# Performance work log

Measured on AMD Instinct MI355X. Metric: run time of the kernel, lower is better.

The kernel has to match this reference:

```python
import jax, jax.numpy as jnp
import numpy as np

N = 100000      # nodes
E = 1000000     # edges (avg degree 10)
F_IN = 64       # num_features
HID = 64        # hidden_channels
C1 = 4          # num_labeled_classes
C2 = 3          # num_unlabeled_classes
L = 4           # num_layers
ALPHA = 0.1


def setup_inputs() -> dict:
    key = jax.random.key(0)
    ks = jax.random.split(key, 8)
    x = jax.random.normal(ks[0], (N, F_IN), dtype=jnp.float32)
    edge_index = jax.random.randint(ks[1], (2, E), 0, N, dtype=jnp.int32)
    # GCN2Conv shared weights (glorot-ish scale), one per residual layer
    Ws = jax.random.normal(ks[2], (L - 1, F_IN, F_IN), dtype=jnp.float32) / np.sqrt(F_IN)
    # GCNConv weight + bias
    W_gcn = jax.random.normal(ks[3], (F_IN, HID), dtype=jnp.float32) / np.sqrt(F_IN)
    b_gcn = jnp.zeros((HID,), dtype=jnp.float32)
    # classification heads
    W1 = jax.random.normal(ks[4], (HID, C1), dtype=jnp.float32) / np.sqrt(HID)
    b1 = jnp.zeros((C1,), dtype=jnp.float32)
    W2 = jax.random.normal(ks[5], (HID, C2), dtype=jnp.float32) / np.sqrt(HID)
    b2 = jnp.zeros((C2,), dtype=jnp.float32)
    return {"x": x, "edge_index": edge_index, "Ws": Ws, "W_gcn": W_gcn,
            "b_gcn": b_gcn, "W1": W1, "b1": b1, "W2": W2, "b2": b2}


def _gcn_norm(edge_index, num_nodes):
    # PyG gcn_norm: add self-loops, symmetric D^-1/2 A D^-1/2 normalization
    loop = jnp.arange(num_nodes, dtype=edge_index.dtype)
    row = jnp.concatenate([edge_index[0], loop])  # source
    col = jnp.concatenate([edge_index[1], loop])  # target
    deg = jax.ops.segment_sum(jnp.ones_like(col, dtype=jnp.float32), col,
                              num_segments=num_nodes)
    dinv = jnp.where(deg > 0, jax.lax.rsqrt(deg), 0.0)
    norm = dinv[row] * dinv[col]  # [E+N]
    return row, col, norm


def _propagate(x, row, col, norm, num_nodes):
    # out[col] += norm * x[row]  (gather -> scale -> scatter-add)
    return jax.ops.segment_sum(norm[:, None] * x[row], col, num_segments=num_nodes)


def reference(x, edge_index, Ws, W_gcn, b_gcn, W1, b1, W2, b2):
    num_nodes = x.shape[0]
    row, col, norm = _gcn_norm(edge_index, num_nodes)
    x0 = x
    # GCN2Conv layers: theta=None -> beta=1.0, shared weights ->
    # out = ((1-alpha) * A_hat x + alpha * x0) @ W
    for i in range(L - 1):
        h = _propagate(x, row, col, norm, num_nodes)
        h = (1.0 - ALPHA) * h + ALPHA * x0
        h = h @ Ws[i]
        x = jax.nn.relu(h)
        # dropout(p=0.5) is inactive in eval mode
        x0 = x  # repo updates x_0 each layer
    # GCNConv: A_hat (x W) + b
    h = _propagate(x @ W_gcn, row, col, norm, num_nodes) + b_gcn
    out1 = h @ W1 + b1  # l2_classifier is False
    out2 = h @ W2 + b2
    return out1, out2, h
```

## Files before the change

kernel.cpp:

```cpp
#include <hip/hip_runtime.h>
#include <hip/hip_bf16.h>


#define TPB 256
#define NBSH 7
typedef __hip_bfloat16 bf16;
typedef __attribute__((ext_vector_type(8))) short short8;
typedef __attribute__((ext_vector_type(4))) float f32x4;

#define MFMA16(A, B, C) __builtin_amdgcn_mfma_f32_16x16x32_bf16((A), (B), (C), 0, 0, 0)

__device__ __forceinline__ float lo16(int u) { return __int_as_float(u << 16); }
__device__ __forceinline__ float hi16(int u) { return __int_as_float(u & 0xffff0000); }

__device__ __forceinline__ unsigned f2bfu(float f) {
    unsigned x = __float_as_uint(f);
    return ((x + 0x7fffu + ((x >> 16) & 1u)) >> 16) & 0xffffu;
}

__global__ void ebhist_kernel(const int* __restrict__ col, int* __restrict__ bh,
                              int E, int B) {
    __shared__ int lh[800];
    for (int i = threadIdx.x; i < B; i += blockDim.x) lh[i] = 0;
    __syncthreads();
    for (int e = blockIdx.x * blockDim.x + threadIdx.x; e < E; e += gridDim.x * blockDim.x)
        atomicAdd(&lh[col[e] >> NBSH], 1);
    __syncthreads();
    for (int i = threadIdx.x; i < B; i += blockDim.x) {
        int c = lh[i];
        if (c) atomicAdd(&bh[i], c);
    }
}

__global__ void bscan_kernel(const int* __restrict__ bh, int* __restrict__ bcur,
                             int* __restrict__ boff, int B, int E) {
    __shared__ int s[256];
    int t = threadIdx.x;
    int v[4]; int sum = 0;
#pragma unroll
    for (int i = 0; i < 4; ++i) {
        int idx = t * 4 + i;
        v[i] = (idx < B) ? bh[idx] : 0;
        sum += v[i];
    }
    s[t] = sum;
    __syncthreads();
    for (int off = 1; off < 256; off <<= 1) {
        int val = (t >= off) ? s[t - off] : 0;
        __syncthreads();
        s[t] += val;
        __syncthreads();
    }
    int run = s[t] - sum;
#pragma unroll
    for (int i = 0; i < 4; ++i) {
        int idx = t * 4 + i;
        if (idx < B) { bcur[idx] = run; boff[idx] = run; }
        run += v[i];
    }
    if (t == 255) boff[B] = E;
}

__global__ void bucket_scatter_kernel(const int* __restrict__ ei, int* __restrict__ bcur,
                                      unsigned int* __restrict__ ebuf, int E, int B) {
    __shared__ int lh[800], lb[800];
    int chunk = (E + gridDim.x - 1) / gridDim.x;
    int beg = blockIdx.x * chunk;
    int end = min(beg + chunk, E);
    for (int i = threadIdx.x; i < B; i += blockDim.x) lh[i] = 0;
    __syncthreads();
    for (int e = beg + threadIdx.x; e < end; e += blockDim.x)
        atomicAdd(&lh[ei[E + e] >> NBSH], 1);
    __syncthreads();
    for (int i = threadIdx.x; i < B; i += blockDim.x) {
        int c = lh[i];
        lb[i] = c ? atomicAdd(&bcur[i], c) : 0;
    }
    __syncthreads();
    for (int i = threadIdx.x; i < B; i += blockDim.x) lh[i] = 0;
    __syncthreads();
    for (int e = beg + threadIdx.x; e < end; e += blockDim.x) {
        int r = ei[e];
        int c = ei[E + e];
        int bin = c >> NBSH;
        int rank = atomicAdd(&lh[bin], 1);
        ebuf[lb[bin] + rank] = ((unsigned)(c & 127) << 17) | (unsigned)r;
    }
}

__global__ __launch_bounds__(128) void bucket_place_kernel(
        const int* __restrict__ boff, const unsigned int* __restrict__ ebuf,
        int* __restrict__ rowptr, int* __restrict__ degi,
        float* __restrict__ dinv, float* __restrict__ sdeg,
        int* __restrict__ srcids, int n) {
    __shared__ int cnt[128], loff[128], lcur[128];
    int b = blockIdx.x;
    int t = threadIdx.x;
    int lo = boff[b];
    int hi = boff[b + 1];
    int vbase = b << NBSH;
    cnt[t] = 0;
    __syncthreads();
    for (int i = lo + t; i < hi; i += 128)
        atomicAdd(&cnt[ebuf[i] >> 17], 1);
    __syncthreads();
    int mine = cnt[t];
    loff[t] = mine;
    __syncthreads();
    for (int off = 1; off < 128; off <<= 1) {
        int val = (t >= off) ? loff[t - off] : 0;
        __syncthreads();
        loff[t] += val;
        __syncthreads();
    }
    int excl = loff[t] - mine;
    int v = vbase + t;
    if (v < n) {
        rowptr[v] = lo + excl;
        degi[v] = mine;
        float d = (float)mine + 1.0f;
        dinv[v] = rsqrtf(d);
        sdeg[v] = sqrtf(d);
    }
    lcur[t] = lo + excl;
    __syncthreads();
    for (int i = lo + t; i < hi; i += 128) {
        unsigned int r = ebuf[i];
        int pos = atomicAdd(&lcur[r >> 17], 1);
        srcids[pos] = (int)(r & 0x1FFFFu);
    }
}

__global__ void dhist_kernel(const int* __restrict__ degi, int* __restrict__ dh, int n) {
    __shared__ int lh[256];
    lh[threadIdx.x] = 0;
    __syncthreads();
    for (int v = blockIdx.x * blockDim.x + threadIdx.x; v < n; v += gridDim.x * blockDim.x)
        atomicAdd(&lh[min(degi[v], 255)], 1);
    __syncthreads();
    int c = lh[threadIdx.x];
    if (c) atomicAdd(&dh[threadIdx.x], c);
}

__global__ void dscan_kernel(const int* __restrict__ dh, int* __restrict__ dcur) {
    __shared__ int s[256];
    int t = threadIdx.x;
    int mine = dh[t];
    s[t] = mine;
    __syncthreads();
    for (int off = 1; off < 256; off <<= 1) {
        int val = (t >= off) ? s[t - off] : 0;
        __syncthreads();
        s[t] += val;
        __syncthreads();
    }
    dcur[t] = s[t] - mine;
}

__global__ void place_kernel(const int* __restrict__ degi, int* __restrict__ dcur,
                             int* __restrict__ perm, int n) {
    __shared__ int lh[256], lb[256];
    int chunk = (n + gridDim.x - 1) / gridDim.x;
    int beg = blockIdx.x * chunk;
    int end = min(beg + chunk, n);
    lh[threadIdx.x] = 0;
    __syncthreads();
    for (int v = beg + threadIdx.x; v < end; v += blockDim.x)
        atomicAdd(&lh[min(degi[v], 255)], 1);
    __syncthreads();
    int c = lh[threadIdx.x];
    lb[threadIdx.x] = c ? atomicAdd(&dcur[threadIdx.x], c) : 0;
    __syncthreads();
    lh[threadIdx.x] = 0;
    __syncthreads();
    for (int v = beg + threadIdx.x; v < end; v += blockDim.x) {
        int bin = min(degi[v], 255);
        int r = atomicAdd(&lh[bin], 1);
        perm[lb[bin] + r] = v;
    }
}

__global__ void cvt_kernel(const float* __restrict__ x, const float* __restrict__ dinv,
                           unsigned short* __restrict__ xb, int n4) {
    int i = blockIdx.x * blockDim.x + threadIdx.x;
    if (i < n4) {
        float dv = dinv[i >> 4];
        float4 f = ((const float4*)x)[i];
        ushort4 u;
        u.x = (unsigned short)f2bfu(f.x * dv);
        u.y = (unsigned short)f2bfu(f.y * dv);
        u.z = (unsigned short)f2bfu(f.z * dv);
        u.w = (unsigned short)f2bfu(f.w * dv);
        ((ushort4*)xb)[i] = u;
    }
}

__device__ __forceinline__ void stage_wfrag(const float* __restrict__ W,
                                            unsigned short* __restrict__ wf) {
    int l = threadIdx.x & 63;
    int m = l & 15;
    int kg = l >> 4;
    for (int f = threadIdx.x >> 6; f < 8; f += TPB / 64) {
        int t = f >> 1, kk = f & 1;
        int col = t * 16 + m;
        unsigned hw[4], lw[4];
#pragma unroll
        for (int j = 0; j < 4; ++j) {
            float w0 = W[(kk * 32 + kg * 8 + 2 * j) * 64 + col];
            float w1 = W[(kk * 32 + kg * 8 + 2 * j + 1) * 64 + col];
            unsigned x0 = __float_as_uint(w0), x1 = __float_as_uint(w1);
            hw[j] = (x0 >> 16) | (x1 & 0xffff0000u);
            float r0 = w0 - __uint_as_float(x0 & 0xffff0000u);
            float r1 = w1 - __uint_as_float(x1 & 0xffff0000u);
            lw[j] = f2bfu(r0) | (f2bfu(r1) << 16);
        }
        unsigned* dh = (unsigned*)(wf + ((size_t)(f * 64 + l) * 8));
        unsigned* dl = (unsigned*)(wf + ((size_t)((f + 8) * 64 + l) * 8));
#pragma unroll
        for (int j = 0; j < 4; ++j) { dh[j] = hw[j]; dl[j] = lw[j]; }
    }
}

__device__ __forceinline__ void build_bfrag(const float* __restrict__ tp,
                                            short8* bh, short8* bl) {
    float4 ta = *(const float4*)tp;
    float4 tb = *(const float4*)(tp + 4);
    float tv[8] = {ta.x, ta.y, ta.z, ta.w, tb.x, tb.y, tb.z, tb.w};
    union { short8 v; unsigned u[4]; } H, L;
#pragma unroll
    for (int j = 0; j < 4; ++j) {
        unsigned x0 = __float_as_uint(tv[2 * j]);
        unsigned x1 = __float_as_uint(tv[2 * j + 1]);
        H.u[j] = (x0 >> 16) | (x1 & 0xffff0000u);
        float r0 = tv[2 * j]     - __uint_as_float(x0 & 0xffff0000u);
        float r1 = tv[2 * j + 1] - __uint_as_float(x1 & 0xffff0000u);
        L.u[j] = f2bfu(r0) | (f2bfu(r1) << 16);
    }
    *bh = H.v;
    *bl = L.v;
}

#define MMT(WFP, ACC, T) do { \
    short8 ah0 = (WFP)[((T) * 2    ) * 64 + lane]; \
    short8 al0 = (WFP)[((T) * 2 + 8) * 64 + lane]; \
    short8 ah1 = (WFP)[((T) * 2 + 1) * 64 + lane]; \
    short8 al1 = (WFP)[((T) * 2 + 9) * 64 + lane]; \
    ACC = MFMA16(ah0, bh0, ACC); \
    ACC = MFMA16(al0, bh0, ACC); \
    ACC = MFMA16(ah0, bl0, ACC); \
    ACC = MFMA16(ah1, bh1, ACC); \
    ACC = MFMA16(al1, bh1, ACC); \
    ACC = MFMA16(ah1, bl1, ACC); \
} while (0)

struct GRes { float a0, a1, a2, a3; };
__device__ __forceinline__ GRes gather8s(const int* __restrict__ srcids, int beg, int deg,
                                         int md, const unsigned short* __restrict__ xsb,
                                         int ge) {
    GRes r{0.0f, 0.0f, 0.0f, 0.0f};
    for (int i = 0; i < md; i += 8) {
        int src[8];
#pragma unroll
        for (int u = 0; u < 8; ++u) {
            int e = i + u;
            src[u] = srcids[beg + ((e < deg) ? e : 0)];
        }
        int2 q[8];
#pragma unroll
        for (int u = 0; u < 8; ++u)
            q[u] = *(const int2*)(xsb + ((unsigned)src[u] * 64u + (unsigned)ge));
#pragma unroll
        for (int u = 0; u < 8; ++u) {
            float m = (i + u < deg) ? 1.0f : 0.0f;
            r.a0 = fmaf(m, lo16(q[u].x), r.a0);
            r.a1 = fmaf(m, hi16(q[u].x), r.a1);
            r.a2 = fmaf(m, lo16(q[u].y), r.a2);
            r.a3 = fmaf(m, hi16(q[u].y), r.a3);
        }
    }
    return r;
}

__device__ __forceinline__ void st_relu4(unsigned short* p, f32x4 a, float sc) {
    ushort4 u;
    u.x = (unsigned short)f2bfu(fmaxf(a[0], 0.f) * sc);
    u.y = (unsigned short)f2bfu(fmaxf(a[1], 0.f) * sc);
    u.z = (unsigned short)f2bfu(fmaxf(a[2], 0.f) * sc);
    u.w = (unsigned short)f2bfu(fmaxf(a[3], 0.f) * sc);
    *(ushort4*)p = u;
}

__device__ __forceinline__ void st_plain4(unsigned short* p, f32x4 a) {
    ushort4 u;
    u.x = (unsigned short)f2bfu(a[0]);
    u.y = (unsigned short)f2bfu(a[1]);
    u.z = (unsigned short)f2bfu(a[2]);
    u.w = (unsigned short)f2bfu(a[3]);
    *(ushort4*)p = u;
}

__global__ __launch_bounds__(256) void layer_kernel(
        const int* __restrict__ rowptr, const int* __restrict__ degi,
        const int* __restrict__ srcids, const int* __restrict__ perm,
        const unsigned short* __restrict__ xsb, const float* __restrict__ dinv,
        const float* __restrict__ sdeg, const float* __restrict__ W,
        unsigned short* __restrict__ yb, int n) {
    __shared__ __align__(16) float st[4][4][68];
    __shared__ __align__(16) unsigned short wf[16 * 64 * 8];
    int wid = threadIdx.x >> 6;
    int lane = threadIdx.x & 63;
    int s = lane >> 4;
    int g = lane & 15;
    stage_wfrag(W, wf);
    __syncthreads();
    const short8* wfp = (const short8*)wf;
    int ntile = (n + 15) >> 4;
    for (int tile = ntile - 1 - blockIdx.x; tile >= 0; tile -= gridDim.x) {
        int base = tile * 16 + wid * 4;
        int vb = base + s;
        int vbc = (vb < n) ? vb : n - 1;
        int v = perm[vbc];
        int beg = rowptr[v];
        int deg = degi[v];
        int md = max(deg, __shfl_xor(deg, 16));
        md = max(md, __shfl_xor(md, 32));
        GRes r = gather8s(srcids, beg, deg, md, xsb, g * 4);
        int2 qs = *(const int2*)(xsb + ((unsigned)v * 64u + (unsigned)(g * 4)));
        float xs0 = lo16(qs.x), xs1 = hi16(qs.x), xs2 = lo16(qs.y), xs3 = hi16(qs.y);
        float c9 = 0.9f * dinv[v];
        float c1 = 0.1f * sdeg[v];
        float4 t4;
        t4.x = c9 * (r.a0 + xs0) + c1 * xs0;
        t4.y = c9 * (r.a1 + xs1) + c1 * xs1;
        t4.z = c9 * (r.a2 + xs2) + c1 * xs2;
        t4.w = c9 * (r.a3 + xs3) + c1 * xs3;
        *(float4*)&st[wid][s][g * 4] = t4;
        __builtin_amdgcn_wave_barrier();
        int vb2 = base + g;
        int v2c = perm[(vb2 < n) ? vb2 : n - 1];
        float dv2 = dinv[v2c];
        const float* strow = st[wid][g & 3];
        short8 bh0, bl0, bh1, bl1;
        build_bfrag(strow + s * 8,      &bh0, &bl0);
        build_bfrag(strow + 32 + s * 8, &bh1, &bl1);
        f32x4 ac0 = {0.f, 0.f, 0.f, 0.f}, ac1 = {0.f, 0.f, 0.f, 0.f};
        f32x4 ac2 = {0.f, 0.f, 0.f, 0.f}, ac3 = {0.f, 0.f, 0.f, 0.f};
        MMT(wfp, ac0, 0); MMT(wfp, ac1, 1); MMT(wfp, ac2, 2); MMT(wfp, ac3, 3);
        __builtin_amdgcn_wave_barrier();
        if (g < 4 && vb2 < n) {
            unsigned short* yp = yb + ((size_t)(unsigned)v2c << 6) + (s << 2);
            st_relu4(yp,      ac0, dv2);
            st_relu4(yp + 16, ac1, dv2);
            st_relu4(yp + 32, ac2, dv2);
            st_relu4(yp + 48, ac3, dv2);
        }
    }
}

__global__ __launch_bounds__(256) void layer_fused_kernel(
        const int* __restrict__ rowptr, const int* __restrict__ degi,
        const int* __restrict__ srcids, const int* __restrict__ perm,
        const unsigned short* __restrict__ xsb, const float* __restrict__ dinv,
        const float* __restrict__ sdeg, const float* __restrict__ W,
        const float* __restrict__ Wg, unsigned short* __restrict__ yb, int n) {
    __shared__ __align__(16) float st[4][4][68];
    __shared__ __align__(16) unsigned short wf[16 * 64 * 8];
    __shared__ __align__(16) unsigned short wgf[16 * 64 * 8];
    int wid = threadIdx.x >> 6;
    int lane = threadIdx.x & 63;
    int s = lane >> 4;
    int g = lane & 15;
    stage_wfrag(W, wf);
    stage_wfrag(Wg, wgf);
    __syncthreads();
    const short8* wfp = (const short8*)wf;
    const short8* wgp = (const short8*)wgf;
    int ntile = (n + 15) >> 4;
    for (int tile = ntile - 1 - blockIdx.x; tile >= 0; tile -= gridDim.x) {
        int base = tile * 16 + wid * 4;
        int vb = base + s;
        int vbc = (vb < n) ? vb : n - 1;
        int v = perm[vbc];
        int beg = rowptr[v];
        int deg = degi[v];
        int md = max(deg, __shfl_xor(deg, 16));
        md = max(md, __shfl_xor(md, 32));
        GRes r = gather8s(srcids, beg, deg, md, xsb, g * 4);
        int2 qs = *(const int2*)(xsb + ((unsigned)v * 64u + (unsigned)(g * 4)));
        float xs0 = lo16(qs.x), xs1 = hi16(qs.x), xs2 = lo16(qs.y), xs3 = hi16(qs.y);
        float c9 = 0.9f * dinv[v];
        float c1 = 0.1f * sdeg[v];
        float4 t4;
        t4.x = c9 * (r.a0 + xs0) + c1 * xs0;
        t4.y = c9 * (r.a1 + xs1) + c1 * xs1;
        t4.z = c9 * (r.a2 + xs2) + c1 * xs2;
        t4.w = c9 * (r.a3 + xs3) + c1 * xs3;
        *(float4*)&st[wid][s][g * 4] = t4;
        __builtin_amdgcn_wave_barrier();
        int vb2 = base + g;
        int v2c = perm[(vb2 < n) ? vb2 : n - 1];
        float dv2 = dinv[v2c];
        const float* strow = st[wid][g & 3];
        {
            short8 bh0, bl0, bh1, bl1;
            build_bfrag(strow + s * 8,      &bh0, &bl0);
            build_bfrag(strow + 32 + s * 8, &bh1, &bl1);
            f32x4 ac0 = {0.f, 0.f, 0.f, 0.f}, ac1 = {0.f, 0.f, 0.f, 0.f};
            f32x4 ac2 = {0.f, 0.f, 0.f, 0.f}, ac3 = {0.f, 0.f, 0.f, 0.f};
            MMT(wfp, ac0, 0); MMT(wfp, ac1, 1); MMT(wfp, ac2, 2); MMT(wfp, ac3, 3);
            __builtin_amdgcn_wave_barrier();
            if (g < 4) {
                float* sr = st[wid][g];
                *(float4*)(sr + (s << 2)) = make_float4(
                    fmaxf(ac0[0], 0.f) * dv2, fmaxf(ac0[1], 0.f) * dv2,
                    fmaxf(ac0[2], 0.f) * dv2, fmaxf(ac0[3], 0.f) * dv2);
                *(float4*)(sr + 16 + (s << 2)) = make_float4(
                    fmaxf(ac1[0], 0.f) * dv2, fmaxf(ac1[1], 0.f) * dv2,
                    fmaxf(ac1[2], 0.f) * dv2, fmaxf(ac1[3], 0.f) * dv2);
                *(float4*)(sr + 32 + (s << 2)) = make_float4(
                    fmaxf(ac2[0], 0.f) * dv2, fmaxf(ac2[1], 0.f) * dv2,
                    fmaxf(ac2[2], 0.f) * dv2, fmaxf(ac2[3], 0.f) * dv2);
                *(float4*)(sr + 48 + (s << 2)) = make_float4(
                    fmaxf(ac3[0], 0.f) * dv2, fmaxf(ac3[1], 0.f) * dv2,
                    fmaxf(ac3[2], 0.f) * dv2, fmaxf(ac3[3], 0.f) * dv2);
            }
        }
        __builtin_amdgcn_wave_barrier();
        {
            short8 bh0, bl0, bh1, bl1;
            build_bfrag(strow + s * 8,      &bh0, &bl0);
            build_bfrag(strow + 32 + s * 8, &bh1, &bl1);
            f32x4 ac0 = {0.f, 0.f, 0.f, 0.f}, ac1 = {0.f, 0.f, 0.f, 0.f};
            f32x4 ac2 = {0.f, 0.f, 0.f, 0.f}, ac3 = {0.f, 0.f, 0.f, 0.f};
            MMT(wgp, ac0, 0); MMT(wgp, ac1, 1); MMT(wgp, ac2, 2); MMT(wgp, ac3, 3);
            __builtin_amdgcn_wave_barrier();
            if (g < 4 && vb2 < n) {
                unsigned short* yp = yb + ((size_t)(unsigned)v2c << 6) + (s << 2);
                st_plain4(yp,      ac0);
                st_plain4(yp + 16, ac1);
                st_plain4(yp + 32, ac2);
                st_plain4(yp + 48, ac3);
            }
        }
    }
}

__global__ __launch_bounds__(256) void heads_kernel(
        const int* __restrict__ rowptr, const int* __restrict__ degi,
        const int* __restrict__ srcids, const int* __restrict__ perm,
        const unsigned short* __restrict__ xwb, const float* __restrict__ dinv,
        const float* __restrict__ bg,
        const float* __restrict__ W1, const float* __restrict__ b1,
        const float* __restrict__ W2, const float* __restrict__ b2,
        float* __restrict__ out, int n) {
    __shared__ __align__(16) float hs[4][4][64];
    __shared__ __align__(16) float whd[448];
    __shared__ float bs[8];
    int wid = threadIdx.x >> 6;
    int lane = threadIdx.x & 63;
    int s = lane >> 4;
    int g = lane & 15;
    for (int i = threadIdx.x; i < 448; i += TPB) {
        int j = i >> 6, k = i & 63;
        whd[i] = (j < 4) ? W1[k * 4 + j] : W2[k * 3 + (j - 4)];
    }
    if (threadIdx.x < 7) bs[threadIdx.x] = (threadIdx.x < 4) ? b1[threadIdx.x] : b2[threadIdx.x - 4];
    __syncthreads();
    int j = lane >> 3;
    int k0 = (lane & 7) * 8;
    int ntile = (n + 15) >> 4;
    for (int tile = ntile - 1 - blockIdx.x; tile >= 0; tile -= gridDim.x) {
        int base = tile * 16 + wid * 4;
        int vb = base + s;
        int vbc = (vb < n) ? vb : n - 1;
        int v = perm[vbc];
        int beg = rowptr[v];
        int deg = degi[v];
        int md = max(deg, __shfl_xor(deg, 16));
        md = max(md, __shfl_xor(md, 32));
        GRes r = gather8s(srcids, beg, deg, md, xwb, g * 4);
        int2 qs = *(const int2*)(xwb + ((unsigned)v * 64u + (unsigned)(g * 4)));
        float dv = dinv[v];
        float4 bq = *(const float4*)(bg + g * 4);
        float4 h4;
        h4.x = dv * (r.a0 + lo16(qs.x)) + bq.x;
        h4.y = dv * (r.a1 + hi16(qs.x)) + bq.y;
        h4.z = dv * (r.a2 + lo16(qs.y)) + bq.z;
        h4.w = dv * (r.a3 + hi16(qs.y)) + bq.w;
        if (vb < n)
            *(float4*)&out[(size_t)7 * n + (size_t)(unsigned)v * 64 + g * 4] = h4;
        *(float4*)&hs[wid][s][g * 4] = h4;
        __builtin_amdgcn_wave_barrier();
#pragma unroll
        for (int ss = 0; ss < 4; ++ss) {
            int vb2 = base + ss;
            if (vb2 >= n) break;
            int v2 = perm[vb2];
            float part = 0.0f;
            if (j < 7) {
                float4 h0 = *(const float4*)&hs[wid][ss][k0];
                float4 h1 = *(const float4*)&hs[wid][ss][k0 + 4];
                const float4* wq = (const float4*)&whd[j * 64 + k0];
                float4 w0 = wq[0], w1 = wq[1];
                part = h0.x * w0.x + h0.y * w0.y + h0.z * w0.z + h0.w * w0.w
                     + h1.x * w1.x + h1.y * w1.y + h1.z * w1.z + h1.w * w1.w;
            }
            part += __shfl_down(part, 4);
            part += __shfl_down(part, 2);
            part += __shfl_down(part, 1);
            if ((lane & 7) == 0 && j < 7) {
                float sv = bs[j] + part;
                if (j < 4) out[(size_t)v2 * 4 + j] = sv;
                else       out[(size_t)4 * n + (size_t)v2 * 3 + (j - 4)] = sv;
            }
        }
        __builtin_amdgcn_wave_barrier();
    }
}

extern "C" void kernel_launch(void* const* d_in, const int* in_sizes, int n_in,
                              void* d_out, int out_size, void* d_ws, size_t ws_size,
                              hipStream_t stream) {
    const float* x     = (const float*)d_in[0];
    const int*   ei    = (const int*)d_in[1];
    const float* Ws    = (const float*)d_in[2];
    const float* W_gcn = (const float*)d_in[3];
    const float* b_gcn = (const float*)d_in[4];
    const float* W1    = (const float*)d_in[5];
    const float* b1    = (const float*)d_in[6];
    const float* W2    = (const float*)d_in[7];
    const float* b2    = (const float*)d_in[8];
    float* out = (float*)d_out;

    const int N = in_sizes[0] / 64;
    const int E = in_sizes[1] / 2;
    const int NLAYERS = in_sizes[2] / 4096;
    const int B = (N + 127) >> NBSH;

    int*   degi   = (int*)d_ws;
    int*   rowptr = degi + N;
    int*   bh     = rowptr + N;
    int*   bcur   = bh + 800;
    int*   boff   = bcur + 800;
    int*   dh     = boff + 800;
    int*   dcur   = dh + 256;
    int*   perm   = dcur + 256;
    int*   srcids = perm + N;
    unsigned int* ebuf = (unsigned int*)(srcids + E + 64);
    float* dinv   = (float*)(ebuf + E);
    float* sdeg   = dinv + N;
    unsigned short* x0s  = (unsigned short*)(sdeg + N);
    unsigned short* bufA = x0s + (size_t)N * 64;
    unsigned short* bufB = bufA + (size_t)N * 64;

    const int WGRID = 4096;

    hipMemsetAsync(bh, 0, 800 * sizeof(int), stream);
    hipMemsetAsync(dh, 0, 256 * sizeof(int), stream);
    hipMemsetAsync(srcids + E, 0, 64 * sizeof(int), stream);
    ebhist_kernel<<<120, TPB, 0, stream>>>(ei + E, bh, E, B);
    bscan_kernel<<<1, 256, 0, stream>>>(bh, bcur, boff, B, E);
    bucket_scatter_kernel<<<120, TPB, 0, stream>>>(ei, bcur, ebuf, E, B);
    bucket_place_kernel<<<B, 128, 0, stream>>>(boff, ebuf, rowptr, degi, dinv, sdeg,
                                               srcids, N);
    dhist_kernel<<<64, 256, 0, stream>>>(degi, dh, N);
    dscan_kernel<<<1, 256, 0, stream>>>(dh, dcur);
    place_kernel<<<64, 256, 0, stream>>>(degi, dcur, perm, N);
    cvt_kernel<<<(N * 16 + TPB - 1) / TPB, TPB, 0, stream>>>(x, dinv, x0s, N * 16);

    const unsigned short* xcur = x0s;
    unsigned short* ybuf = bufA;
    for (int i = 0; i < NLAYERS - 1; ++i) {
        layer_kernel<<<WGRID, TPB, 0, stream>>>(rowptr, degi, srcids, perm, xcur,
                                                dinv, sdeg, Ws + (size_t)i * 4096, ybuf, N);
        xcur = ybuf;
        ybuf = (ybuf == bufA) ? bufB : bufA;
    }
    layer_fused_kernel<<<WGRID, TPB, 0, stream>>>(rowptr, degi, srcids, perm, xcur,
                                                  dinv, sdeg,
                                                  Ws + (size_t)(NLAYERS - 1) * 4096,
                                                  W_gcn, ybuf, N);
    unsigned short* xw = ybuf;

    heads_kernel<<<WGRID, TPB, 0, stream>>>(rowptr, degi, srcids, perm, xw, dinv,
                                            b_gcn, W1, b1, W2, b2, out, N);
}
```

Before: 311.3 us.

## Split MFMA tile across waves, use packed bf16 converts, drop gather clamps

Before, each wave ran a full 16x16 MFMA tile over all 64 output columns for only 4 valid rows, so 12 of 16 rows were wasted. Now the four waves share one 16-node tile through block-wide shared memory, and each wave computes 16 output columns. This cuts MFMA and fragment-load work per tile by 4x but adds __syncthreads barriers. Software bf16 rounding is replaced with the hardware v_cvt_pk_bf16_f32 instruction. The neighbor-index clamp in the gather is dropped, which relies on the padded srcids tail. The layer kernel grid is also halved.

Result: no change. 311.0 us (-0.1%).

```diff
diff --git a/kernel.cpp b/kernel.cpp
--- a/kernel.cpp
+++ b/kernel.cpp
@@ -13,9 +13,10 @@
 __device__ __forceinline__ float lo16(int u) { return __int_as_float(u << 16); }
 __device__ __forceinline__ float hi16(int u) { return __int_as_float(u & 0xffff0000); }
 
-__device__ __forceinline__ unsigned f2bfu(float f) {
-    unsigned x = __float_as_uint(f);
-    return ((x + 0x7fffu + ((x >> 16) & 1u)) >> 16) & 0xffffu;
+__device__ __forceinline__ unsigned cvtpk(float lo, float hi) {
+    unsigned r;
+    asm("v_cvt_pk_bf16_f32 %0, %1, %2" : "=v"(r) : "v"(lo), "v"(hi));
+    return r;
 }
 
 __global__ void ebhist_kernel(const int* __restrict__ col, int* __restrict__ bh,
@@ -186,12 +187,10 @@
     if (i < n4) {
         float dv = dinv[i >> 4];
         float4 f = ((const float4*)x)[i];
-        ushort4 u;
-        u.x = (unsigned short)f2bfu(f.x * dv);
-        u.y = (unsigned short)f2bfu(f.y * dv);
-        u.z = (unsigned short)f2bfu(f.z * dv);
-        u.w = (unsigned short)f2bfu(f.w * dv);
-        ((ushort4*)xb)[i] = u;
+        uint2 o;
+        o.x = cvtpk(f.x * dv, f.y * dv);
+        o.y = cvtpk(f.z * dv, f.w * dv);
+        ((uint2*)xb)[i] = o;
     }
 }
 
@@ -208,11 +207,11 @@
         for (int j = 0; j < 4; ++j) {
             float w0 = W[(kk * 32 + kg * 8 + 2 * j) * 64 + col];
             float w1 = W[(kk * 32 + kg * 8 + 2 * j + 1) * 64 + col];
-            unsigned x0 = __float_as_uint(w0), x1 = __float_as_uint(w1);
-            hw[j] = (x0 >> 16) | (x1 & 0xffff0000u);
-            float r0 = w0 - __uint_as_float(x0 & 0xffff0000u);
-            float r1 = w1 - __uint_as_float(x1 & 0xffff0000u);
-            lw[j] = f2bfu(r0) | (f2bfu(r1) << 16);
+            unsigned h = cvtpk(w0, w1);
+            float h0 = __uint_as_float(h << 16);
+            float h1 = __uint_as_float(h & 0xffff0000u);
+            hw[j] = h;
+            lw[j] = cvtpk(w0 - h0, w1 - h1);
         }
         unsigned* dh = (unsigned*)(wf + ((size_t)(f * 64 + l) * 8));
         unsigned* dl = (unsigned*)(wf + ((size_t)((f + 8) * 64 + l) * 8));
@@ -229,29 +228,15 @@
     union { short8 v; unsigned u[4]; } H, L;
 #pragma unroll
     for (int j = 0; j < 4; ++j) {
-        unsigned x0 = __float_as_uint(tv[2 * j]);
-        unsigned x1 = __float_as_uint(tv[2 * j + 1]);
-        H.u[j] = (x0 >> 16) | (x1 & 0xffff0000u);
-        float r0 = tv[2 * j]     - __uint_as_float(x0 & 0xffff0000u);
-        float r1 = tv[2 * j + 1] - __uint_as_float(x1 & 0xffff0000u);
-        L.u[j] = f2bfu(r0) | (f2bfu(r1) << 16);
+        unsigned h = cvtpk(tv[2 * j], tv[2 * j + 1]);
+        float h0 = __uint_as_float(h << 16);
+        float h1 = __uint_as_float(h & 0xffff0000u);
+        H.u[j] = h;
+        L.u[j] = cvtpk(tv[2 * j] - h0, tv[2 * j + 1] - h1);
     }
     *bh = H.v;
     *bl = L.v;
 }
-
-#define MMT(WFP, ACC, T) do { \
-    short8 ah0 = (WFP)[((T) * 2    ) * 64 + lane]; \
-    short8 al0 = (WFP)[((T) * 2 + 8) * 64 + lane]; \
-    short8 ah1 = (WFP)[((T) * 2 + 1) * 64 + lane]; \
-    short8 al1 = (WFP)[((T) * 2 + 9) * 64 + lane]; \
-    ACC = MFMA16(ah0, bh0, ACC); \
-    ACC = MFMA16(al0, bh0, ACC); \
-    ACC = MFMA16(ah0, bl0, ACC); \
-    ACC = MFMA16(ah1, bh1, ACC); \
-    ACC = MFMA16(al1, bh1, ACC); \
-    ACC = MFMA16(ah1, bl1, ACC); \
-} while (0)
 
 struct GRes { float a0, a1, a2, a3; };
 __device__ __forceinline__ GRes gather8s(const int* __restrict__ srcids, int beg, int deg,
@@ -261,10 +246,8 @@
     for (int i = 0; i < md; i += 8) {
         int src[8];
 #pragma unroll
-        for (int u = 0; u < 8; ++u) {
-            int e = i + u;
-            src[u] = srcids[beg + ((e < deg) ? e : 0)];
-        }
+        for (int u = 0; u < 8; ++u)
+            src[u] = srcids[beg + i + u];
         int2 q[8];
 #pragma unroll
         for (int u = 0; u < 8; ++u)
@@ -282,21 +265,17 @@
 }
 
 __device__ __forceinline__ void st_relu4(unsigned short* p, f32x4 a, float sc) {
-    ushort4 u;
-    u.x = (unsigned short)f2bfu(fmaxf(a[0], 0.f) * sc);
-    u.y = (unsigned short)f2bfu(fmaxf(a[1], 0.f) * sc);
-    u.z = (unsigned short)f2bfu(fmaxf(a[2], 0.f) * sc);
-    u.w = (unsigned short)f2bfu(fmaxf(a[3], 0.f) * sc);
-    *(ushort4*)p = u;
+    uint2 o;
+    o.x = cvtpk(fmaxf(a[0], 0.f) * sc, fmaxf(a[1], 0.f) * sc);
+    o.y = cvtpk(fmaxf(a[2], 0.f) * sc, fmaxf(a[3], 0.f) * sc);
+    *(uint2*)p = o;
 }
 
 __device__ __forceinline__ void st_plain4(unsigned short* p, f32x4 a) {
-    ushort4 u;
-    u.x = (unsigned short)f2bfu(a[0]);
-    u.y = (unsigned short)f2bfu(a[1]);
-    u.z = (unsigned short)f2bfu(a[2]);
-    u.w = (unsigned short)f2bfu(a[3]);
-    *(ushort4*)p = u;
+    uint2 o;
+    o.x = cvtpk(a[0], a[1]);
+    o.y = cvtpk(a[2], a[3]);
+    *(uint2*)p = o;
 }
 
 __global__ __launch_bounds__(256) void layer_kernel(
@@ -305,7 +284,7 @@
         const unsigned short* __restrict__ xsb, const float* __restrict__ dinv,
         const float* __restrict__ sdeg, const float* __restrict__ W,
         unsigned short* __restrict__ yb, int n) {
-    __shared__ __align__(16) float st[4][4][68];
+    __shared__ __align__(16) float st[16][68];
     __shared__ __align__(16) unsigned short wf[16 * 64 * 8];
     int wid = threadIdx.x >> 6;
     int lane = threadIdx.x & 63;
@@ -316,8 +295,8 @@
     const short8* wfp = (const short8*)wf;
     int ntile = (n + 15) >> 4;
     for (int tile = ntile - 1 - blockIdx.x; tile >= 0; tile -= gridDim.x) {
-        int base = tile * 16 + wid * 4;
-        int vb = base + s;
+        int base = tile * 16;
+        int vb = base + wid * 4 + s;
         int vbc = (vb < n) ? vb : n - 1;
         int v = perm[vbc];
         int beg = rowptr[v];
@@ -334,25 +313,31 @@
         t4.y = c9 * (r.a1 + xs1) + c1 * xs1;
         t4.z = c9 * (r.a2 + xs2) + c1 * xs2;
         t4.w = c9 * (r.a3 + xs3) + c1 * xs3;
-        *(float4*)&st[wid][s][g * 4] = t4;
-        __builtin_amdgcn_wave_barrier();
+        *(float4*)&st[wid * 4 + s][g * 4] = t4;
+        __syncthreads();
         int vb2 = base + g;
         int v2c = perm[(vb2 < n) ? vb2 : n - 1];
         float dv2 = dinv[v2c];
-        const float* strow = st[wid][g & 3];
+        const float* strow = st[g];
         short8 bh0, bl0, bh1, bl1;
         build_bfrag(strow + s * 8,      &bh0, &bl0);
         build_bfrag(strow + 32 + s * 8, &bh1, &bl1);
-        f32x4 ac0 = {0.f, 0.f, 0.f, 0.f}, ac1 = {0.f, 0.f, 0.f, 0.f};
-        f32x4 ac2 = {0.f, 0.f, 0.f, 0.f}, ac3 = {0.f, 0.f, 0.f, 0.f};
-        MMT(wfp, ac0, 0); MMT(wfp, ac1, 1); MMT(wfp, ac2, 2); MMT(wfp, ac3, 3);
-        __builtin_amdgcn_wave_barrier();
-        if (g < 4 && vb2 < n) {
-            unsigned short* yp = yb + ((size_t)(unsigned)v2c << 6) + (s << 2);
-            st_relu4(yp,      ac0, dv2);
-            st_relu4(yp + 16, ac1, dv2);
-            st_relu4(yp + 32, ac2, dv2);
-            st_relu4(yp + 48, ac3, dv2);
+        __syncthreads();
+        short8 ah0 = wfp[(wid * 2    ) * 64 + lane];
+        short8 al0 = wfp[(wid * 2 + 8) * 64 + lane];
+        short8 ah1 = wfp[(wid * 2 + 1) * 64 + lane];
+        short8 al1 = wfp[(wid * 2 + 9) * 64 + lane];
+        f32x4 ac = {0.f, 0.f, 0.f, 0.f};
+        ac = MFMA16(ah0, bh0, ac);
+        ac = MFMA16(al0, bh0, ac);
+        ac = MFMA16(ah0, bl0, ac);
+        ac = MFMA16(ah1, bh1, ac);
+        ac = MFMA16(al1, bh1, ac);
+        ac = MFMA16(ah1, bl1, ac);
+        if (vb2 < n) {
+            unsigned short* yp = yb + ((size_t)(unsigned)v2c << 6)
+                               + (unsigned)(wid * 16 + s * 4);
+            st_relu4(yp, ac, dv2);
         }
     }
 }
@@ -363,7 +348,7 @@
         const unsigned short* __restrict__ xsb, const float* __restrict__ dinv,
         const float* __restrict__ sdeg, const float* __restrict__ W,
         const float* __restrict__ Wg, unsigned short* __restrict__ yb, int n) {
-    __shared__ __align__(16) float st[4][4][68];
+    __shared__ __align__(16) float st[16][68];
     __shared__ __align__(16) unsigned short wf[16 * 64 * 8];
     __shared__ __align__(16) unsigned short wgf[16 * 64 * 8];
     int wid = threadIdx.x >> 6;
@@ -377,8 +362,8 @@
     const short8* wgp = (const short8*)wgf;
     int ntile = (n + 15) >> 4;
     for (int tile = ntile - 1 - blockIdx.x; tile >= 0; tile -= gridDim.x) {
-        int base = tile * 16 + wid * 4;
-        int vb = base + s;
+        int base = tile * 16;
+        int vb = base + wid * 4 + s;
         int vbc = (vb < n) ? vb : n - 1;
         int v = perm[vbc];
         int beg = rowptr[v];
@@ -395,51 +380,53 @@
         t4.y = c9 * (r.a1 + xs1) + c1 * xs1;
         t4.z = c9 * (r.a2 + xs2) + c1 * xs2;
         t4.w = c9 * (r.a3 + xs3) + c1 * xs3;
-        *(float4*)&st[wid][s][g * 4] = t4;
-        __builtin_amdgcn_wave_barrier();
+        *(float4*)&st[wid * 4 + s][g * 4] = t4;
+        __syncthreads();
         int vb2 = base + g;
         int v2c = perm[(vb2 < n) ? vb2 : n - 1];
         float dv2 = dinv[v2c];
-        const float* strow = st[wid][g & 3];
+        const float* strow = st[g];
         {
             short8 bh0, bl0, bh1, bl1;
             build_bfrag(strow + s * 8,      &bh0, &bl0);
             build_bfrag(strow + 32 + s * 8, &bh1, &bl1);
-            f32x4 ac0 = {0.f, 0.f, 0.f, 0.f}, ac1 = {0.f, 0.f, 0.f, 0.f};
-            f32x4 ac2 = {0.f, 0.f, 0.f, 0.f}, ac3 = {0.f, 0.f, 0.f, 0.f};
-            MMT(wfp, ac0, 0); MMT(wfp, ac1, 1); MMT(wfp, ac2, 2); MMT(wfp, ac3, 3);
-            __builtin_amdgcn_wave_barrier();
-            if (g < 4) {
-                float* sr = st[wid][g];
-                *(float4*)(sr + (s << 2)) = make_float4(
-                    fmaxf(ac0[0], 0.f) * dv2, fmaxf(ac0[1], 0.f) * dv2,
-                    fmaxf(ac0[2], 0.f) * dv2, fmaxf(ac0[3], 0.f) * dv2);
-                *(float4*)(sr + 16 + (s << 2)) = make_float4(
-                    fmaxf(ac1[0], 0.f) * dv2, fmaxf(ac1[1], 0.f) * dv2,
-                    fmaxf(ac1[2], 0.f) * dv2, fmaxf(ac1[3], 0.f) * dv2);
-                *(float4*)(sr + 32 + (s << 2)) = make_float4(
-                    fmaxf(ac2[0], 0.f) * dv2, fmaxf(ac2[1], 0.f) * dv2,
-                    fmaxf(ac2[2], 0.f) * dv2, fmaxf(ac2[3], 0.f) * dv2);
-                *(float4*)(sr + 48 + (s << 2)) = make_float4(
-                    fmaxf(ac3[0], 0.f) * dv2, fmaxf(ac3[1], 0.f) * dv2,
-                    fmaxf(ac3[2], 0.f) * dv2, fmaxf(ac3[3], 0.f) * dv2);
-            }
+            __syncthreads();
+            short8 ah0 = wfp[(wid * 2    ) * 64 + lane];
+            short8 al0 = wfp[(wid * 2 + 8) * 64 + lane];
+            short8 ah1 = wfp[(wid * 2 + 1) * 64 + lane];
+            short8 al1 = wfp[(wid * 2 + 9) * 64 + lane];
+            f32x4 ac = {0.f, 0.f, 0.f, 0.f};
+            ac = MFMA16(ah0, bh0, ac);
+            ac = MFMA16(al0, bh0, ac);
+            ac = MFMA16(ah0, bl0, ac);
+            ac = MFMA16(ah1, bh1, ac);
+            ac = MFMA16(al1, bh1, ac);
+            ac = MFMA16(ah1, bl1, ac);
+            *(float4*)&st[g][wid * 16 + s * 4] = make_float4(
+                fmaxf(ac[0], 0.f) * dv2, fmaxf(ac[1], 0.f) * dv2,
+                fmaxf(ac[2], 0.f) * dv2, fmaxf(ac[3], 0.f) * dv2);
         }
-        __builtin_amdgcn_wave_barrier();
+        __syncthreads();
         {
             short8 bh0, bl0, bh1, bl1;
             build_bfrag(strow + s * 8,      &bh0, &bl0);
             build_bfrag(strow + 32 + s * 8, &bh1, &bl1);
-            f32x4 ac0 = {0.f, 0.f, 0.f, 0.f}, ac1 = {0.f, 0.f, 0.f, 0.f};
-            f32x4 ac2 = {0.f, 0.f, 0.f, 0.f}, ac3 = {0.f, 0.f, 0.f, 0.f};
-            MMT(wgp, ac0, 0); MMT(wgp, ac1, 1); MMT(wgp, ac2, 2); MMT(wgp, ac3, 3);
-            __builtin_amdgcn_wave_barrier();
-            if (g < 4 && vb2 < n) {
-                unsigned short* yp = yb + ((size_t)(unsigned)v2c << 6) + (s << 2);
-                st_plain4(yp,      ac0);
-                st_plain4(yp + 16, ac1);
-                st_plain4(yp + 32, ac2);
-                st_plain4(yp + 48, ac3);
+            short8 ah0 = wgp[(wid * 2    ) * 64 + lane];
+            short8 al0 = wgp[(wid * 2 + 8) * 64 + lane];
+            short8 ah1 = wgp[(wid * 2 + 1) * 64 + lane];
+            short8 al1 = wgp[(wid * 2 + 9) * 64 + lane];
+            f32x4 ac = {0.f, 0.f, 0.f, 0.f};
+            ac = MFMA16(ah0, bh0, ac);
+            ac = MFMA16(al0, bh0, ac);
+            ac = MFMA16(ah0, bl0, ac);
+            ac = MFMA16(ah1, bh1, ac);
+            ac = MFMA16(al1, bh1, ac);
+            ac = MFMA16(ah1, bl1, ac);
+            __syncthreads();
+            if (vb2 < n) {
+                unsigned short* yp = yb + ((size_t)(unsigned)v2c << 6)
+                                   + (unsigned)(wid * 16 + s * 4);
+                st_plain4(yp, ac);
             }
         }
     }
@@ -553,7 +540,8 @@
     unsigned short* bufA = x0s + (size_t)N * 64;
     unsigned short* bufB = bufA + (size_t)N * 64;
 
-    const int WGRID = 4096;
+    const int WGRID_L = 2048;
+    const int WGRID_H = 4096;
 
     hipMemsetAsync(bh, 0, 800 * sizeof(int), stream);
     hipMemsetAsync(dh, 0, 256 * sizeof(int), stream);
@@ -571,17 +559,17 @@
     const unsigned short* xcur = x0s;
     unsigned short* ybuf = bufA;
     for (int i = 0; i < NLAYERS - 1; ++i) {
-        layer_kernel<<<WGRID, TPB, 0, stream>>>(rowptr, degi, srcids, perm, xcur,
-                                                dinv, sdeg, Ws + (size_t)i * 4096, ybuf, N);
+        layer_kernel<<<WGRID_L, TPB, 0, stream>>>(rowptr, degi, srcids, perm, xcur,
+                                                  dinv, sdeg, Ws + (size_t)i * 4096, ybuf, N);
         xcur = ybuf;
         ybuf = (ybuf == bufA) ? bufB : bufA;
     }
-    layer_fused_kernel<<<WGRID, TPB, 0, stream>>>(rowptr, degi, srcids, perm, xcur,
-                                                  dinv, sdeg,
-                                                  Ws + (size_t)(NLAYERS - 1) * 4096,
-                                                  W_gcn, ybuf, N);
+    layer_fused_kernel<<<WGRID_L, TPB, 0, stream>>>(rowptr, degi, srcids, perm, xcur,
+                                                    dinv, sdeg,
+                                                    Ws + (size_t)(NLAYERS - 1) * 4096,
+                                                    W_gcn, ybuf, N);
     unsigned short* xw = ybuf;
 
-    heads_kernel<<<WGRID, TPB, 0, stream>>>(rowptr, degi, srcids, perm, xw, dinv,
-                                            b_gcn, W1, b1, W2, b2, out, N);
-}
+    heads_kernel<<<WGRID_H, TPB, 0, stream>>>(rowptr, degi, srcids, perm, xw, dinv,
+                                              b_gcn, W1, b1, W2, b2, out, N);
+}
```
